# Optimization experiments

Hardware: AMD Instinct MI355X
Metric: run time of the kernel (lower is better)

Reference implementation:

```python
import jax, jax.numpy as jnp
import numpy as np

T = 20.0
SCALE = 0.3


def setup_inputs() -> dict:
    key = jax.random.key(0)
    ks = jax.random.split(key, 6)
    B, C = 16384, 1000
    inp = {f"outputs{i+1}": jax.random.normal(ks[i], (B, C), dtype=jnp.float32) for i in range(5)}
    inp["targets"] = jax.random.randint(ks[5], (B,), 0, C, dtype=jnp.int64)
    return inp


def reference(outputs1, outputs2, outputs3, outputs4, outputs5, targets):
    # [5, B, C] stacked softmax predictions at temperature T
    preds = jnp.stack([outputs1, outputs2, outputs3, outputs4, outputs5], axis=0)
    preds = jax.nn.softmax(preds / T, axis=-1)
    # center over class dim and L2-normalize -> Pearson correlation via dot product
    v = preds - jnp.mean(preds, axis=-1, keepdims=True)            # [M,B,C]
    v = v / jnp.sqrt(jnp.sum(v * v, axis=-1, keepdims=True))       # [M,B,C]
    corr = jnp.einsum("mbc,nbc->mnb", v, v)                        # [M,M,B]
    M = preds.shape[0]
    iu, ju = jnp.triu_indices(M, k=1)
    d = jnp.sum(corr[iu, ju, :], axis=0)                            # [B] sum over pairs
    return jnp.mean(SCALE * d)
```

## Files before the change

kernel.cpp:

```cpp
#include <hip/hip_runtime.h>


typedef float f32x4 __attribute__((ext_vector_type(4)));

#define CDIM   1000
#define C4DIM  250
#define NM     5
#define NP     15
#define T_INV  (1.0f / 20.0f)
#define SCALEF 0.3f

#define GLOAD(dst, p) \
    asm volatile("global_load_dwordx4 %0, %1, off" : "=v"(dst) : "v"(p) : "memory")

#define WAITVM(N)                                              \
    asm volatile("s_waitcnt vmcnt(" #N ")" ::: "memory");      \
    __builtin_amdgcn_sched_barrier(0)

template <bool MASKED>
__device__ __forceinline__ void slot_accum(const f32x4* xs, bool act,
                                           float* A, float* Bv)
{
    float u[NM][4];
    #pragma unroll
    for (int m = 0; m < NM; ++m) {
        #pragma unroll
        for (int c = 0; c < 4; ++c) {
            float xv = xs[m][c];
            if (MASKED) xv = act ? xv : 0.0f;
            u[m][c] = __expf(xv * T_INV) - 1.0f;
        }
    }
    #pragma unroll
    for (int c = 0; c < 4; ++c) {
        #pragma unroll
        for (int i = 0; i < NM; ++i) A[i] += u[i][c];
        int p = 0;
        #pragma unroll
        for (int i = 0; i < NM; ++i) {
            #pragma unroll
            for (int j = i; j < NM; ++j) {
                Bv[p] = fmaf(u[i][c], u[j][c], Bv[p]);
                ++p;
            }
        }
    }
}

__global__ __launch_bounds__(256) void diversity_rows(
    const float* __restrict__ o1, const float* __restrict__ o2,
    const float* __restrict__ o3, const float* __restrict__ o4,
    const float* __restrict__ o5, float* __restrict__ ws, int B)
{
    const int lane = threadIdx.x & 63;
    const int wid  = threadIdx.x >> 6;
    const int b    = blockIdx.x * 4 + wid;
    if (b >= B) return;

    const bool act3 = (lane + 192) < C4DIM;
    const int  i3   = act3 ? (lane + 192) : (C4DIM - 1);

    const size_t roff = (size_t)b * CDIM;
    const float* rp[NM] = {o1 + roff, o2 + roff, o3 + roff, o4 + roff, o5 + roff};

    f32x4 x0[NM], x1[NM], x2[NM], x3[NM];
    #pragma unroll
    for (int m = 0; m < NM; ++m) GLOAD(x0[m], rp[m] + (size_t)lane * 4);
    #pragma unroll
    for (int m = 0; m < NM; ++m) GLOAD(x1[m], rp[m] + (size_t)(lane + 64) * 4);
    #pragma unroll
    for (int m = 0; m < NM; ++m) GLOAD(x2[m], rp[m] + (size_t)(lane + 128) * 4);
    #pragma unroll
    for (int m = 0; m < NM; ++m) GLOAD(x3[m], rp[m] + (size_t)i3 * 4);

    float A[NM], Bv[NP];
    #pragma unroll
    for (int i = 0; i < NM; ++i) A[i] = 0.0f;
    #pragma unroll
    for (int p = 0; p < NP; ++p) Bv[p] = 0.0f;

    WAITVM(15);  slot_accum<false>(x0, true, A, Bv);
    WAITVM(10);  slot_accum<false>(x1, true, A, Bv);
    WAITVM(5);   slot_accum<false>(x2, true, A, Bv);
    WAITVM(0);   slot_accum<true >(x3, act3, A, Bv);

    #pragma unroll
    for (int off = 32; off >= 1; off >>= 1) {
        #pragma unroll
        for (int i = 0; i < NM; ++i) A[i] += __shfl_xor(A[i], off);
        #pragma unroll
        for (int p = 0; p < NP; ++p) Bv[p] += __shfl_xor(Bv[p], off);
    }

    {
        const float Cf = (float)CDIM;
        const int diag[NM] = {0, 5, 9, 12, 14};
        float rden[NM];
        #pragma unroll
        for (int i = 0; i < NM; ++i)
            rden[i] = rsqrtf(fmaf(Cf, Bv[diag[i]], -A[i] * A[i]));

        float d = 0.0f;
        int p = 0;
        #pragma unroll
        for (int i = 0; i < NM; ++i) {
            #pragma unroll
            for (int j = i; j < NM; ++j) {
                if (j > i)
                    d += fmaf(Cf, Bv[p], -A[i] * A[j]) * rden[i] * rden[j];
                ++p;
            }
        }
        if (lane == 0)
            ws[b] = SCALEF * d;
    }
}

__global__ __launch_bounds__(1024) void final_reduce(
    const float* __restrict__ ws, float* __restrict__ out, int B)
{
    __shared__ double sm[1024];
    double acc = 0.0;
    for (int i = threadIdx.x; i < B; i += 1024)
        acc += (double)ws[i];
    sm[threadIdx.x] = acc;
    __syncthreads();
    #pragma unroll
    for (int s = 512; s > 0; s >>= 1) {
        if (threadIdx.x < s) sm[threadIdx.x] += sm[threadIdx.x + s];
        __syncthreads();
    }
    if (threadIdx.x == 0)
        out[0] = (float)(sm[0] / (double)B);
}

extern "C" void kernel_launch(void* const* d_in, const int* in_sizes, int n_in,
                              void* d_out, int out_size, void* d_ws, size_t ws_size,
                              hipStream_t stream)
{
    const float* o1 = (const float*)d_in[0];
    const float* o2 = (const float*)d_in[1];
    const float* o3 = (const float*)d_in[2];
    const float* o4 = (const float*)d_in[3];
    const float* o5 = (const float*)d_in[4];

    float* ws  = (float*)d_ws;
    float* out = (float*)d_out;

    const int B = in_sizes[0] / CDIM;

    diversity_rows<<<(B + 3) / 4, 256, 0, stream>>>(o1, o2, o3, o4, o5, ws, B);
    final_reduce<<<1, 1024, 0, stream>>>(ws, out, B);
}
```

Before: 64.29 us.

## Process four rows per wave and pre-reduce per block before final reduce

Each wave now loops over four consecutive rows instead of one, accumulating the per-row diversity into a register, and each block writes one partial sum through shared memory. The final reduce shrinks to 256 threads over the per-block partials. This cuts the grid size and the size of the second-stage reduction. The row loop is not unrolled and waits for all loads before computing, so there is no cross-row prefetch; memory-level parallelism per wave may drop. The loop also assumes B is a multiple of ROWS, since there is no per-row bounds check.

New measurement: 63.44 us. No clear change (-1.3%).

```diff
diff --git a/kernel.cpp b/kernel.cpp
--- a/kernel.cpp
+++ b/kernel.cpp
@@ -7,6 +7,7 @@
 #define C4DIM  250
 #define NM     5
 #define NP     15
+#define ROWS   4
 #define T_INV  (1.0f / 20.0f)
 #define SCALEF 0.3f
 
@@ -16,6 +17,19 @@
 #define WAITVM(N)                                              \
     asm volatile("s_waitcnt vmcnt(" #N ")" ::: "memory");      \
     __builtin_amdgcn_sched_barrier(0)
+
+__device__ __forceinline__ void issue_row(const float* const* rp, int lane, int i3,
+                                          f32x4* x0, f32x4* x1, f32x4* x2, f32x4* x3)
+{
+    #pragma unroll
+    for (int m = 0; m < NM; ++m) GLOAD(x0[m], rp[m] + (size_t)lane * 4);
+    #pragma unroll
+    for (int m = 0; m < NM; ++m) GLOAD(x1[m], rp[m] + (size_t)(lane + 64) * 4);
+    #pragma unroll
+    for (int m = 0; m < NM; ++m) GLOAD(x2[m], rp[m] + (size_t)(lane + 128) * 4);
+    #pragma unroll
+    for (int m = 0; m < NM; ++m) GLOAD(x3[m], rp[m] + (size_t)i3 * 4);
+}
 
 template <bool MASKED>
 __device__ __forceinline__ void slot_accum(const f32x4* xs, bool act,
@@ -54,79 +68,89 @@
 {
     const int lane = threadIdx.x & 63;
     const int wid  = threadIdx.x >> 6;
-    const int b    = blockIdx.x * 4 + wid;
-    if (b >= B) return;
+    const int b0   = (blockIdx.x * 4 + wid) * ROWS;
+
+    __shared__ float sm4[4];
 
     const bool act3 = (lane + 192) < C4DIM;
     const int  i3   = act3 ? (lane + 192) : (C4DIM - 1);
 
-    const size_t roff = (size_t)b * CDIM;
-    const float* rp[NM] = {o1 + roff, o2 + roff, o3 + roff, o4 + roff, o5 + roff};
+    float dsum = 0.0f;
 
-    f32x4 x0[NM], x1[NM], x2[NM], x3[NM];
-    #pragma unroll
-    for (int m = 0; m < NM; ++m) GLOAD(x0[m], rp[m] + (size_t)lane * 4);
-    #pragma unroll
-    for (int m = 0; m < NM; ++m) GLOAD(x1[m], rp[m] + (size_t)(lane + 64) * 4);
-    #pragma unroll
-    for (int m = 0; m < NM; ++m) GLOAD(x2[m], rp[m] + (size_t)(lane + 128) * 4);
-    #pragma unroll
-    for (int m = 0; m < NM; ++m) GLOAD(x3[m], rp[m] + (size_t)i3 * 4);
+    if (b0 < B) {
+        const float* rp[NM] = {
+            o1 + (size_t)b0 * CDIM, o2 + (size_t)b0 * CDIM, o3 + (size_t)b0 * CDIM,
+            o4 + (size_t)b0 * CDIM, o5 + (size_t)b0 * CDIM};
 
-    float A[NM], Bv[NP];
-    #pragma unroll
-    for (int i = 0; i < NM; ++i) A[i] = 0.0f;
-    #pragma unroll
-    for (int p = 0; p < NP; ++p) Bv[p] = 0.0f;
+        #pragma unroll 1
+        for (int r = 0; r < ROWS; ++r) {
+            f32x4 x0[NM], x1[NM], x2[NM], x3[NM];
+            issue_row(rp, lane, i3, x0, x1, x2, x3);
 
-    WAITVM(15);  slot_accum<false>(x0, true, A, Bv);
-    WAITVM(10);  slot_accum<false>(x1, true, A, Bv);
-    WAITVM(5);   slot_accum<false>(x2, true, A, Bv);
-    WAITVM(0);   slot_accum<true >(x3, act3, A, Bv);
+            float A[NM], Bv[NP];
+            #pragma unroll
+            for (int i = 0; i < NM; ++i) A[i] = 0.0f;
+            #pragma unroll
+            for (int p = 0; p < NP; ++p) Bv[p] = 0.0f;
 
-    #pragma unroll
-    for (int off = 32; off >= 1; off >>= 1) {
-        #pragma unroll
-        for (int i = 0; i < NM; ++i) A[i] += __shfl_xor(A[i], off);
-        #pragma unroll
-        for (int p = 0; p < NP; ++p) Bv[p] += __shfl_xor(Bv[p], off);
+            WAITVM(15);  slot_accum<false>(x0, true, A, Bv);
+            WAITVM(10);  slot_accum<false>(x1, true, A, Bv);
+            WAITVM(5);   slot_accum<false>(x2, true, A, Bv);
+            WAITVM(0);   slot_accum<true >(x3, act3, A, Bv);
+            __builtin_amdgcn_sched_barrier(0);
+
+            #pragma unroll
+            for (int off = 32; off >= 1; off >>= 1) {
+                #pragma unroll
+                for (int i = 0; i < NM; ++i) A[i] += __shfl_xor(A[i], off);
+                #pragma unroll
+                for (int p = 0; p < NP; ++p) Bv[p] += __shfl_xor(Bv[p], off);
+            }
+
+            {
+                const float Cf = (float)CDIM;
+                const int diag[NM] = {0, 5, 9, 12, 14};
+                float rden[NM];
+                #pragma unroll
+                for (int i = 0; i < NM; ++i)
+                    rden[i] = rsqrtf(fmaf(Cf, Bv[diag[i]], -A[i] * A[i]));
+
+                float d = 0.0f;
+                int p = 0;
+                #pragma unroll
+                for (int i = 0; i < NM; ++i) {
+                    #pragma unroll
+                    for (int j = i; j < NM; ++j) {
+                        if (j > i)
+                            d += fmaf(Cf, Bv[p], -A[i] * A[j]) * rden[i] * rden[j];
+                        ++p;
+                    }
+                }
+                dsum += SCALEF * d;
+            }
+
+            #pragma unroll
+            for (int m = 0; m < NM; ++m) rp[m] += CDIM;
+        }
     }
 
-    {
-        const float Cf = (float)CDIM;
-        const int diag[NM] = {0, 5, 9, 12, 14};
-        float rden[NM];
-        #pragma unroll
-        for (int i = 0; i < NM; ++i)
-            rden[i] = rsqrtf(fmaf(Cf, Bv[diag[i]], -A[i] * A[i]));
-
-        float d = 0.0f;
-        int p = 0;
-        #pragma unroll
-        for (int i = 0; i < NM; ++i) {
-            #pragma unroll
-            for (int j = i; j < NM; ++j) {
-                if (j > i)
-                    d += fmaf(Cf, Bv[p], -A[i] * A[j]) * rden[i] * rden[j];
-                ++p;
-            }
-        }
-        if (lane == 0)
-            ws[b] = SCALEF * d;
-    }
+    if (lane == 0) sm4[wid] = dsum;
+    __syncthreads();
+    if (threadIdx.x == 0)
+        ws[blockIdx.x] = (sm4[0] + sm4[1]) + (sm4[2] + sm4[3]);
 }
 
-__global__ __launch_bounds__(1024) void final_reduce(
-    const float* __restrict__ ws, float* __restrict__ out, int B)
+__global__ __launch_bounds__(256) void final_reduce(
+    const float* __restrict__ ws, float* __restrict__ out, int nblk, int B)
 {
-    __shared__ double sm[1024];
+    __shared__ double sm[256];
     double acc = 0.0;
-    for (int i = threadIdx.x; i < B; i += 1024)
+    for (int i = threadIdx.x; i < nblk; i += 256)
         acc += (double)ws[i];
     sm[threadIdx.x] = acc;
     __syncthreads();
     #pragma unroll
-    for (int s = 512; s > 0; s >>= 1) {
+    for (int s = 128; s > 0; s >>= 1) {
         if (threadIdx.x < s) sm[threadIdx.x] += sm[threadIdx.x + s];
         __syncthreads();
     }
@@ -148,7 +172,9 @@
     float* out = (float*)d_out;
 
     const int B = in_sizes[0] / CDIM;
+    const int waves  = (B + ROWS - 1) / ROWS;
+    const int blocks = (waves + 3) / 4;
 
-    diversity_rows<<<(B + 3) / 4, 256, 0, stream>>>(o1, o2, o3, o4, o5, ws, B);
-    final_reduce<<<1, 1024, 0, stream>>>(ws, out, B);
+    diversity_rows<<<blocks, 256, 0, stream>>>(o1, o2, o3, o4, o5, ws, B);
+    final_reduce<<<1, 256, 0, stream>>>(ws, out, blocks, B);
 }
```
